# Performance work log

Measured on AMD Instinct MI355X. Metric: run time of the kernel, lower is better.

## Reference

```python
import jax, jax.numpy as jnp
import numpy as np

B, N, K, H, HEADS = 4, 2000, 30, 128, 4
D = H // HEADS  # per-head dim = 32
NUM_IN = 2 * H
NEG_INF = jnp.float32(np.finfo(np.float32).min)


def setup_inputs() -> dict:
    key = jax.random.key(0)
    ks = jax.random.split(key, 10)
    h_V = jax.random.normal(ks[0], (B, N, H), jnp.float32)
    h_EV = jax.random.normal(ks[1], (B, N, K, NUM_IN), jnp.float32)
    h_KV = jax.random.normal(ks[2], (B, N, K, H), jnp.float32)
    h_KE = jax.random.normal(ks[3], (B, N, K, H), jnp.float32)
    mask_attend = (jax.random.uniform(ks[4], (B, N, K)) > 0.2).astype(jnp.float32)
    s = 1.0 / np.sqrt(H)
    W_Q = jax.random.normal(ks[5], (H, H), jnp.float32) * s
    W_K1 = jax.random.normal(ks[6], (H, H), jnp.float32) * s
    W_K2 = jax.random.normal(ks[7], (H, H), jnp.float32) * s
    W_V = jax.random.normal(ks[8], (H, NUM_IN), jnp.float32) * (1.0 / np.sqrt(NUM_IN))
    W_O = jax.random.normal(ks[9], (H, H), jnp.float32) * s
    return {"h_V": h_V, "h_EV": h_EV, "h_KV": h_KV, "h_KE": h_KE,
            "mask_attend": mask_attend, "W_Q": W_Q, "W_K1": W_K1,
            "W_K2": W_K2, "W_V": W_V, "W_O": W_O}


def reference(h_V, h_EV, h_KV, h_KE, mask_attend, W_Q, W_K1, W_K2, W_V, W_O):
    # Projections (torch Linear: y = x @ W.T)
    Q = (h_V @ W_Q.T).reshape(B, N, 1, HEADS, D)          # broadcast over K
    K1 = (h_KE @ W_K1.T).reshape(B, N, K, HEADS, D)
    K2 = (h_KV @ W_K2.T).reshape(B, N, K, HEADS, D)
    V = (h_EV @ W_V.T).reshape(B, N, K, HEADS, D)
    # Trilinear score: sum_d Q*K1*K2 -> [B,N,K,h] -> [B,N,h,K], scaled by 1/d
    logits = jnp.einsum('bnkhd,bnkhd->bnkh', Q * K1, K2)
    logits = jnp.transpose(logits, (0, 1, 3, 2)) / D      # [B,N,h,K]
    # Masked softmax over neighbor axis
    mask = jnp.broadcast_to(mask_attend[:, :, None, :], logits.shape)
    logits = jnp.where(mask > 0, logits, NEG_INF)
    attend = jax.nn.softmax(logits, axis=-1) * mask       # [B,N,h,K]
    # Weighted aggregation over neighbors
    h_upd = jnp.einsum('bnhk,bnkhd->bnhd', attend, V).reshape(B, N, H)
    return h_upd @ W_O.T
```

## Files before the change

kernel.cpp:

```cpp
#include <hip/hip_runtime.h>


#define BB 4
#define NNTOK 2000
#define KNB 30
#define HH 128
#define NHEADS 4
#define DDIM 32
#define NUMIN 256
#define TOK (BB*NNTOK)
#define TB 2
#define NBLK (TOK/TB)
#define SAW 136

typedef __bf16 bf16x8 __attribute__((ext_vector_type(8)));
typedef __bf16 bf16x4_t __attribute__((ext_vector_type(4)));
typedef float f32x4 __attribute__((ext_vector_type(4)));

__global__ __launch_bounds__(256) void conv_w_kernel(
    const float* __restrict__ wk1, const float* __restrict__ wk2,
    const float* __restrict__ wv, __bf16* __restrict__ ws) {
  int i = blockIdx.x * 256 + threadIdx.x;
  int e = i * 4;
  const float* src;
  int off;
  if (e < 16384)      { src = wk1; off = e; }
  else if (e < 32768) { src = wk2; off = e - 16384; }
  else                { src = wv;  off = e - 32768; }
  float4 v = *(const float4*)(src + off);
  bf16x4_t o4;
  o4.x = (__bf16)v.x; o4.y = (__bf16)v.y; o4.z = (__bf16)v.z; o4.w = (__bf16)v.w;
  *(bf16x4_t*)(ws + e) = o4;
}

__global__ __launch_bounds__(256, 4) void na_main_kernel(
    const float* __restrict__ h_V, const float* __restrict__ h_EV,
    const float* __restrict__ h_KV, const float* __restrict__ h_KE,
    const float* __restrict__ maskp, const float* __restrict__ W_Q,
    const float* __restrict__ W_O, const __bf16* __restrict__ bW,
    float* __restrict__ out) {
  __shared__ __bf16 sA[64 * SAW];
  __shared__ __bf16 sKP[64 * SAW];
  __shared__ float sQ[TB][HH];
  __shared__ float sLog[TB][NHEADS][32];
  __shared__ float sMask[TB][32];

  const int tid = threadIdx.x;
  const int lane = tid & 63;
  const int wave = tid >> 6;
  const int m = lane & 15;
  const int quad = lane >> 4;
  const int t0 = blockIdx.x * TB;

  const __bf16* bWK1 = bW;
  const __bf16* bWK2 = bW + 16384;
  const __bf16* bWV  = bW + 32768;

  for (int i = tid; i < TB * KNB; i += 256)
    sMask[i / KNB][i % KNB] = maskp[(long)(t0 + i / KNB) * KNB + i % KNB];
  for (int i = tid; i < 4 * SAW; i += 256)
    sA[60 * SAW + i] = (__bf16)0.f;
  {
    const int t = tid >> 7, o = tid & 127;
    const float4* wq = (const float4*)(W_Q + o * HH);
    const float4* hv = (const float4*)(h_V + (long)(t0 + t) * HH);
    float acc = 0.f;
#pragma unroll
    for (int j = 0; j < 32; j++) {
      float4 a = hv[j], b = wq[j];
      acc += a.x * b.x + a.y * b.y + a.z * b.z + a.w * b.w;
    }
    sQ[t][o] = acc;
  }

  auto stage = [&](const float* gsrc, int grs) {
    for (int i = tid; i < 60 * 32; i += 256) {
      int r = i >> 5, c = (i & 31) << 2;
      float4 v = *(const float4*)(gsrc + (long)r * grs + c);
      bf16x4_t o4;
      o4.x = (__bf16)v.x; o4.y = (__bf16)v.y; o4.z = (__bf16)v.z; o4.w = (__bf16)v.w;
      *(bf16x4_t*)&sA[r * SAW + c] = o4;
    }
  };

  f32x4 acc[4][2];
  const f32x4 fzero = {0.f, 0.f, 0.f, 0.f};
  auto zacc = [&]() {
#pragma unroll
    for (int mt = 0; mt < 4; mt++) { acc[mt][0] = fzero; acc[mt][1] = fzero; }
  };
  auto gemm = [&](const __bf16* gW, int ldw, int kb) {
#pragma unroll
    for (int ks = 0; ks < 4; ks++) {
      const int kc = kb + ks * 32 + quad * 8;
      bf16x8 b0 = *(const bf16x8*)(gW + (wave * 32 + m) * ldw + kc);
      bf16x8 b1 = *(const bf16x8*)(gW + (wave * 32 + 16 + m) * ldw + kc);
#pragma unroll
      for (int mt = 0; mt < 4; mt++) {
        bf16x8 a = *(const bf16x8*)&sA[(mt * 16 + m) * SAW + ks * 32 + quad * 8];
        acc[mt][0] = __builtin_amdgcn_mfma_f32_16x16x32_bf16(a, b0, acc[mt][0], 0, 0, 0);
        acc[mt][1] = __builtin_amdgcn_mfma_f32_16x16x32_bf16(a, b1, acc[mt][1], 0, 0, 0);
      }
    }
  };

  __syncthreads();

  stage(h_KE + (long)t0 * KNB * HH, HH);
  __syncthreads();
  zacc();
  gemm(bWK1, HH, 0);
#pragma unroll
  for (int mt = 0; mt < 4; mt++)
#pragma unroll
    for (int nt = 0; nt < 2; nt++)
#pragma unroll
      for (int r = 0; r < 4; r++)
        sKP[(mt * 16 + quad * 4 + r) * SAW + wave * 32 + nt * 16 + m] =
            (__bf16)acc[mt][nt][r];
  __syncthreads();

  stage(h_KV + (long)t0 * KNB * HH, HH);
  __syncthreads();
  zacc();
  gemm(bWK2, HH, 0);
#pragma unroll
  for (int mt = 0; mt < 4; mt++)
#pragma unroll
    for (int nt = 0; nt < 2; nt++)
#pragma unroll
      for (int r = 0; r < 4; r++) {
        int idx = (mt * 16 + quad * 4 + r) * SAW + wave * 32 + nt * 16 + m;
        sKP[idx] = (__bf16)((float)sKP[idx] * acc[mt][nt][r]);
      }
  __syncthreads();

  if (tid < TB * NHEADS * KNB) {
    int t = tid / (NHEADS * KNB), rem = tid % (NHEADS * KNB);
    int h = rem / KNB, k = rem % KNB;
    const __bf16* p = &sKP[(t * KNB + k) * SAW + h * DDIM];
    const float* q = &sQ[t][h * DDIM];
    float s = 0.f;
#pragma unroll
    for (int d = 0; d < DDIM; d++) s += q[d] * (float)p[d];
    sLog[t][h][k] = s * (1.f / DDIM);
  }
  __syncthreads();

  if (tid < TB * NHEADS) {
    int t = tid >> 2, h = tid & 3;
    float mx = -3.4e38f;
    for (int k = 0; k < KNB; k++)
      if (sMask[t][k] > 0.f) mx = fmaxf(mx, sLog[t][h][k]);
    float s = 0.f;
    for (int k = 0; k < KNB; k++) {
      float e = (sMask[t][k] > 0.f) ? __expf(sLog[t][h][k] - mx) : 0.f;
      sLog[t][h][k] = e;
      s += e;
    }
    float inv = (s > 0.f) ? 1.f / s : 0.f;
    for (int k = 0; k < KNB; k++) sLog[t][h][k] *= inv;
  }
  __syncthreads();

  zacc();
  stage(h_EV + (long)t0 * KNB * NUMIN, NUMIN);
  __syncthreads();
  gemm(bWV, NUMIN, 0);
  __syncthreads();
  stage(h_EV + (long)t0 * KNB * NUMIN + 128, NUMIN);
  __syncthreads();
  gemm(bWV, NUMIN, 128);
#pragma unroll
  for (int mt = 0; mt < 4; mt++)
#pragma unroll
    for (int nt = 0; nt < 2; nt++)
#pragma unroll
      for (int r = 0; r < 4; r++)
        sKP[(mt * 16 + quad * 4 + r) * SAW + wave * 32 + nt * 16 + m] =
            (__bf16)acc[mt][nt][r];
  __syncthreads();

  {
    const int t = tid >> 7, c = tid & 127, h = c >> 5;
    float a = 0.f;
#pragma unroll
    for (int k = 0; k < KNB; k++)
      a += sLog[t][h][k] * (float)sKP[(t * KNB + k) * SAW + c];
    sQ[t][c] = a;
  }
  __syncthreads();

  {
    const int t = tid >> 7, o = tid & 127;
    const float4* wo = (const float4*)(W_O + o * HH);
    const float4* u = (const float4*)&sQ[t][0];
    float r = 0.f;
#pragma unroll
    for (int j = 0; j < 32; j++) {
      float4 a = u[j], b = wo[j];
      r += a.x * b.x + a.y * b.y + a.z * b.z + a.w * b.w;
    }
    out[(long)(t0 + t) * HH + o] = r;
  }
}

extern "C" void kernel_launch(void* const* d_in, const int* in_sizes, int n_in,
                              void* d_out, int out_size, void* d_ws, size_t ws_size,
                              hipStream_t stream) {
  const float* h_V  = (const float*)d_in[0];
  const float* h_EV = (const float*)d_in[1];
  const float* h_KV = (const float*)d_in[2];
  const float* h_KE = (const float*)d_in[3];
  const float* mask = (const float*)d_in[4];
  const float* W_Q  = (const float*)d_in[5];
  const float* W_K1 = (const float*)d_in[6];
  const float* W_K2 = (const float*)d_in[7];
  const float* W_V  = (const float*)d_in[8];
  const float* W_O  = (const float*)d_in[9];
  __bf16* bW = (__bf16*)d_ws;

  conv_w_kernel<<<64, 256, 0, stream>>>(W_K1, W_K2, W_V, bW);
  na_main_kernel<<<NBLK, 256, 0, stream>>>(h_V, h_EV, h_KV, h_KE, mask,
                                           W_Q, W_O, bW, (float*)d_out);
}
```

Baseline: 643.8 us.

## Double-buffer staging with register prefetch and compute attention in MFMA registers

Stage tiles through registers into a double-buffered LDS array, so the global load of the next input (KV, then EV halves) is issued before the current GEMM runs. The K1*K2 product, logits, masked softmax and attention-weighted sum of V are now computed directly on the MFMA accumulator registers using cross-lane shuffles, instead of writing bf16 intermediates to LDS and reducing them with a few threads. This removes several __syncthreads, the LDS round trips and the single-thread serial softmax. In exchange it raises register pressure (8 float4 prefetch registers plus two accumulator sets), which may reduce occupancy under the 4-block launch bound, and it clamps out-of-range rows at the tensor end.

After: 628.2 us. -2.4%, faster.

```diff
diff --git a/kernel.cpp b/kernel.cpp
--- a/kernel.cpp
+++ b/kernel.cpp
@@ -1,14 +1,11 @@
 #include <hip/hip_runtime.h>
 
 
-#define BB 4
-#define NNTOK 2000
 #define KNB 30
 #define HH 128
-#define NHEADS 4
-#define DDIM 32
 #define NUMIN 256
-#define TOK (BB*NNTOK)
+#define TOK 8000
+#define TOTROW (TOK*KNB)
 #define TB 2
 #define NBLK (TOK/TB)
 #define SAW 136
@@ -20,10 +17,8 @@
 __global__ __launch_bounds__(256) void conv_w_kernel(
     const float* __restrict__ wk1, const float* __restrict__ wk2,
     const float* __restrict__ wv, __bf16* __restrict__ ws) {
-  int i = blockIdx.x * 256 + threadIdx.x;
-  int e = i * 4;
-  const float* src;
-  int off;
+  int e = (blockIdx.x * 256 + threadIdx.x) * 4;
+  const float* src; int off;
   if (e < 16384)      { src = wk1; off = e; }
   else if (e < 32768) { src = wk2; off = e - 16384; }
   else                { src = wv;  off = e - 32768; }
@@ -39,10 +34,9 @@
     const float* __restrict__ maskp, const float* __restrict__ W_Q,
     const float* __restrict__ W_O, const __bf16* __restrict__ bW,
     float* __restrict__ out) {
-  __shared__ __bf16 sA[64 * SAW];
-  __shared__ __bf16 sKP[64 * SAW];
+  __shared__ __bf16 sA[2][64 * SAW];
   __shared__ float sQ[TB][HH];
-  __shared__ float sLog[TB][NHEADS][32];
+  __shared__ float sU[TB][HH];
   __shared__ float sMask[TB][32];
 
   const int tid = threadIdx.x;
@@ -56,10 +50,50 @@
   const __bf16* bWK2 = bW + 16384;
   const __bf16* bWV  = bW + 32768;
 
-  for (int i = tid; i < TB * KNB; i += 256)
-    sMask[i / KNB][i % KNB] = maskp[(long)(t0 + i / KNB) * KNB + i % KNB];
-  for (int i = tid; i < 4 * SAW; i += 256)
-    sA[60 * SAW + i] = (__bf16)0.f;
+  const int srow = tid >> 5;
+  const int scol = (tid & 31) << 2;
+  float4 sv[8];
+  const long r0 = (long)t0 * KNB + srow;
+
+  auto stage_load = [&](const float* base, int ld, int coloff) {
+#pragma unroll
+    for (int j = 0; j < 8; j++) {
+      long rr = r0 + j * 8;
+      if (rr > TOTROW - 1) rr = TOTROW - 1;
+      sv[j] = *(const float4*)(base + rr * ld + coloff + scol);
+    }
+  };
+  auto stage_store = [&](int b) {
+#pragma unroll
+    for (int j = 0; j < 8; j++) {
+      bf16x4_t o;
+      o.x = (__bf16)sv[j].x; o.y = (__bf16)sv[j].y;
+      o.z = (__bf16)sv[j].z; o.w = (__bf16)sv[j].w;
+      *(bf16x4_t*)&sA[b][(srow + j * 8) * SAW + scol] = o;
+    }
+  };
+
+  f32x4 accA[4][2], accB[4][2];
+  const f32x4 fzero = {0.f, 0.f, 0.f, 0.f};
+  auto gemm = [&](const __bf16* gW, int ldw, int kb, const __bf16* Ab,
+                  f32x4 (*acc)[2]) {
+#pragma unroll
+    for (int ks = 0; ks < 4; ks++) {
+      const int kc = kb + ks * 32 + quad * 8;
+      bf16x8 b0 = *(const bf16x8*)(gW + (wave * 32 + m) * ldw + kc);
+      bf16x8 b1 = *(const bf16x8*)(gW + (wave * 32 + 16 + m) * ldw + kc);
+#pragma unroll
+      for (int mt = 0; mt < 4; mt++) {
+        bf16x8 a = *(const bf16x8*)&Ab[(mt * 16 + m) * SAW + ks * 32 + quad * 8];
+        acc[mt][0] = __builtin_amdgcn_mfma_f32_16x16x32_bf16(a, b0, acc[mt][0], 0, 0, 0);
+        acc[mt][1] = __builtin_amdgcn_mfma_f32_16x16x32_bf16(a, b1, acc[mt][1], 0, 0, 0);
+      }
+    }
+  };
+
+  stage_load(h_KE, HH, 0);
+  if (tid < TB * KNB)
+    sMask[tid / KNB][tid % KNB] = maskp[(long)t0 * KNB + tid];
   {
     const int t = tid >> 7, o = tid & 127;
     const float4* wq = (const float4*)(W_Q + o * HH);
@@ -72,129 +106,138 @@
     }
     sQ[t][o] = acc;
   }
-
-  auto stage = [&](const float* gsrc, int grs) {
-    for (int i = tid; i < 60 * 32; i += 256) {
-      int r = i >> 5, c = (i & 31) << 2;
-      float4 v = *(const float4*)(gsrc + (long)r * grs + c);
-      bf16x4_t o4;
-      o4.x = (__bf16)v.x; o4.y = (__bf16)v.y; o4.z = (__bf16)v.z; o4.w = (__bf16)v.w;
-      *(bf16x4_t*)&sA[r * SAW + c] = o4;
-    }
-  };
-
-  f32x4 acc[4][2];
-  const f32x4 fzero = {0.f, 0.f, 0.f, 0.f};
-  auto zacc = [&]() {
-#pragma unroll
-    for (int mt = 0; mt < 4; mt++) { acc[mt][0] = fzero; acc[mt][1] = fzero; }
-  };
-  auto gemm = [&](const __bf16* gW, int ldw, int kb) {
-#pragma unroll
-    for (int ks = 0; ks < 4; ks++) {
-      const int kc = kb + ks * 32 + quad * 8;
-      bf16x8 b0 = *(const bf16x8*)(gW + (wave * 32 + m) * ldw + kc);
-      bf16x8 b1 = *(const bf16x8*)(gW + (wave * 32 + 16 + m) * ldw + kc);
-#pragma unroll
-      for (int mt = 0; mt < 4; mt++) {
-        bf16x8 a = *(const bf16x8*)&sA[(mt * 16 + m) * SAW + ks * 32 + quad * 8];
-        acc[mt][0] = __builtin_amdgcn_mfma_f32_16x16x32_bf16(a, b0, acc[mt][0], 0, 0, 0);
-        acc[mt][1] = __builtin_amdgcn_mfma_f32_16x16x32_bf16(a, b1, acc[mt][1], 0, 0, 0);
+  stage_store(0);
+  __syncthreads();
+
+  stage_load(h_KV, HH, 0);
+#pragma unroll
+  for (int mt = 0; mt < 4; mt++) { accA[mt][0] = fzero; accA[mt][1] = fzero; }
+  gemm(bWK1, HH, 0, sA[0], accA);
+  stage_store(1);
+  __syncthreads();
+
+#pragma unroll
+  for (int mt = 0; mt < 4; mt++) { accB[mt][0] = fzero; accB[mt][1] = fzero; }
+  gemm(bWK2, HH, 0, sA[1], accB);
+#pragma unroll
+  for (int mt = 0; mt < 4; mt++) {
+    accA[mt][0] *= accB[mt][0];
+    accA[mt][1] *= accB[mt][1];
+  }
+
+  stage_load(h_EV, NUMIN, 0);
+
+  float q0[2], q1[2];
+#pragma unroll
+  for (int nt = 0; nt < 2; nt++) {
+    q0[nt] = sQ[0][wave * 32 + nt * 16 + m];
+    q1[nt] = sQ[1][wave * 32 + nt * 16 + m];
+  }
+  float lg[4][4];
+#pragma unroll
+  for (int mt = 0; mt < 4; mt++)
+#pragma unroll
+    for (int r = 0; r < 4; r++) {
+      int R = mt * 16 + quad * 4 + r;
+      float qa0 = (R < 30) ? q0[0] : q1[0];
+      float qa1 = (R < 30) ? q0[1] : q1[1];
+      lg[mt][r] = accA[mt][0][r] * qa0 + accA[mt][1][r] * qa1;
+    }
+#pragma unroll
+  for (int d = 1; d < 16; d <<= 1)
+#pragma unroll
+    for (int mt = 0; mt < 4; mt++)
+#pragma unroll
+      for (int r = 0; r < 4; r++)
+        lg[mt][r] += __shfl_xor(lg[mt][r], d);
+
+  float mx0 = -3.0e38f, mx1 = -3.0e38f;
+#pragma unroll
+  for (int mt = 0; mt < 4; mt++)
+#pragma unroll
+    for (int r = 0; r < 4; r++) {
+      int R = mt * 16 + quad * 4 + r;
+      if (R < 60) {
+        int t = R >= 30, k = R - 30 * t;
+        float l = (sMask[t][k] > 0.f) ? lg[mt][r] * 0.03125f : -3.0e38f;
+        lg[mt][r] = l;
+        if (t == 0) mx0 = fmaxf(mx0, l); else mx1 = fmaxf(mx1, l);
+      } else lg[mt][r] = -3.0e38f;
+    }
+  mx0 = fmaxf(mx0, __shfl_xor(mx0, 16)); mx0 = fmaxf(mx0, __shfl_xor(mx0, 32));
+  mx1 = fmaxf(mx1, __shfl_xor(mx1, 16)); mx1 = fmaxf(mx1, __shfl_xor(mx1, 32));
+  float s0 = 0.f, s1 = 0.f;
+  float at[4][4];
+#pragma unroll
+  for (int mt = 0; mt < 4; mt++)
+#pragma unroll
+    for (int r = 0; r < 4; r++) {
+      int R = mt * 16 + quad * 4 + r;
+      float e = 0.f;
+      if (R < 60) {
+        int t = R >= 30, k = R - 30 * t;
+        if (sMask[t][k] > 0.f) {
+          float mxt = (t == 0) ? mx0 : mx1;
+          e = __expf(lg[mt][r] - mxt);
+        }
+        if (t == 0) s0 += e; else s1 += e;
       }
-    }
-  };
-
-  __syncthreads();
-
-  stage(h_KE + (long)t0 * KNB * HH, HH);
-  __syncthreads();
-  zacc();
-  gemm(bWK1, HH, 0);
-#pragma unroll
-  for (int mt = 0; mt < 4; mt++)
-#pragma unroll
-    for (int nt = 0; nt < 2; nt++)
-#pragma unroll
-      for (int r = 0; r < 4; r++)
-        sKP[(mt * 16 + quad * 4 + r) * SAW + wave * 32 + nt * 16 + m] =
-            (__bf16)acc[mt][nt][r];
-  __syncthreads();
-
-  stage(h_KV + (long)t0 * KNB * HH, HH);
-  __syncthreads();
-  zacc();
-  gemm(bWK2, HH, 0);
-#pragma unroll
-  for (int mt = 0; mt < 4; mt++)
-#pragma unroll
-    for (int nt = 0; nt < 2; nt++)
-#pragma unroll
-      for (int r = 0; r < 4; r++) {
-        int idx = (mt * 16 + quad * 4 + r) * SAW + wave * 32 + nt * 16 + m;
-        sKP[idx] = (__bf16)((float)sKP[idx] * acc[mt][nt][r]);
+      at[mt][r] = e;
+    }
+  s0 += __shfl_xor(s0, 16); s0 += __shfl_xor(s0, 32);
+  s1 += __shfl_xor(s1, 16); s1 += __shfl_xor(s1, 32);
+  float inv0 = (s0 > 0.f) ? 1.f / s0 : 0.f;
+  float inv1 = (s1 > 0.f) ? 1.f / s1 : 0.f;
+#pragma unroll
+  for (int mt = 0; mt < 4; mt++)
+#pragma unroll
+    for (int r = 0; r < 4; r++) {
+      int R = mt * 16 + quad * 4 + r;
+      at[mt][r] *= (R < 30) ? inv0 : inv1;
+    }
+
+  stage_store(0);
+  __syncthreads();
+
+  stage_load(h_EV, NUMIN, 128);
+#pragma unroll
+  for (int mt = 0; mt < 4; mt++) { accB[mt][0] = fzero; accB[mt][1] = fzero; }
+  gemm(bWV, NUMIN, 0, sA[0], accB);
+  stage_store(1);
+  __syncthreads();
+
+  gemm(bWV, NUMIN, 128, sA[1], accB);
+
+  float u00 = 0.f, u01 = 0.f, u10 = 0.f, u11 = 0.f;
+#pragma unroll
+  for (int mt = 0; mt < 4; mt++)
+#pragma unroll
+    for (int r = 0; r < 4; r++) {
+      int R = mt * 16 + quad * 4 + r;
+      if (R < 30) {
+        u00 += at[mt][r] * accB[mt][0][r];
+        u01 += at[mt][r] * accB[mt][1][r];
+      } else if (R < 60) {
+        u10 += at[mt][r] * accB[mt][0][r];
+        u11 += at[mt][r] * accB[mt][1][r];
       }
-  __syncthreads();
-
-  if (tid < TB * NHEADS * KNB) {
-    int t = tid / (NHEADS * KNB), rem = tid % (NHEADS * KNB);
-    int h = rem / KNB, k = rem % KNB;
-    const __bf16* p = &sKP[(t * KNB + k) * SAW + h * DDIM];
-    const float* q = &sQ[t][h * DDIM];
-    float s = 0.f;
-#pragma unroll
-    for (int d = 0; d < DDIM; d++) s += q[d] * (float)p[d];
-    sLog[t][h][k] = s * (1.f / DDIM);
-  }
-  __syncthreads();
-
-  if (tid < TB * NHEADS) {
-    int t = tid >> 2, h = tid & 3;
-    float mx = -3.4e38f;
-    for (int k = 0; k < KNB; k++)
-      if (sMask[t][k] > 0.f) mx = fmaxf(mx, sLog[t][h][k]);
-    float s = 0.f;
-    for (int k = 0; k < KNB; k++) {
-      float e = (sMask[t][k] > 0.f) ? __expf(sLog[t][h][k] - mx) : 0.f;
-      sLog[t][h][k] = e;
-      s += e;
-    }
-    float inv = (s > 0.f) ? 1.f / s : 0.f;
-    for (int k = 0; k < KNB; k++) sLog[t][h][k] *= inv;
-  }
-  __syncthreads();
-
-  zacc();
-  stage(h_EV + (long)t0 * KNB * NUMIN, NUMIN);
-  __syncthreads();
-  gemm(bWV, NUMIN, 0);
-  __syncthreads();
-  stage(h_EV + (long)t0 * KNB * NUMIN + 128, NUMIN);
-  __syncthreads();
-  gemm(bWV, NUMIN, 128);
-#pragma unroll
-  for (int mt = 0; mt < 4; mt++)
-#pragma unroll
-    for (int nt = 0; nt < 2; nt++)
-#pragma unroll
-      for (int r = 0; r < 4; r++)
-        sKP[(mt * 16 + quad * 4 + r) * SAW + wave * 32 + nt * 16 + m] =
-            (__bf16)acc[mt][nt][r];
-  __syncthreads();
-
-  {
-    const int t = tid >> 7, c = tid & 127, h = c >> 5;
-    float a = 0.f;
-#pragma unroll
-    for (int k = 0; k < KNB; k++)
-      a += sLog[t][h][k] * (float)sKP[(t * KNB + k) * SAW + c];
-    sQ[t][c] = a;
+    }
+  u00 += __shfl_xor(u00, 16); u00 += __shfl_xor(u00, 32);
+  u01 += __shfl_xor(u01, 16); u01 += __shfl_xor(u01, 32);
+  u10 += __shfl_xor(u10, 16); u10 += __shfl_xor(u10, 32);
+  u11 += __shfl_xor(u11, 16); u11 += __shfl_xor(u11, 32);
+  if (quad == 0) {
+    sU[0][wave * 32 + m]      = u00;
+    sU[0][wave * 32 + 16 + m] = u01;
+    sU[1][wave * 32 + m]      = u10;
+    sU[1][wave * 32 + 16 + m] = u11;
   }
   __syncthreads();
 
   {
     const int t = tid >> 7, o = tid & 127;
     const float4* wo = (const float4*)(W_O + o * HH);
-    const float4* u = (const float4*)&sQ[t][0];
+    const float4* u = (const float4*)&sU[t][0];
     float r = 0.f;
 #pragma unroll
     for (int j = 0; j < 32; j++) {
```
